# Kernel optimization log

Hardware: AMD Instinct MI355X
Metric: run time of the kernel (lower is better)

The kernel has to match this reference:

```python
import jax, jax.numpy as jnp
import numpy as np

N_HEADS = 16
NEG_INF = -1e30  # stand-in for -inf, safe in fp32/bf16


def setup_inputs() -> dict:
    key = jax.random.key(0)
    k1, k2, k3, k4 = jax.random.split(key, 4)
    B, T, C = 8, 1024, 1024
    x = jax.random.normal(k1, (B, T, C), dtype=jnp.float32)
    # torch nn.Linear weight layout: [out_features, in_features]
    w_attn = jax.random.normal(k2, (3 * C, C), dtype=jnp.float32) * 0.02
    w_proj = jax.random.normal(k3, (C, C), dtype=jnp.float32) * 0.02
    b_proj = jax.random.normal(k4, (C,), dtype=jnp.float32) * 0.02
    return {"x": x, "w_attn": w_attn, "w_proj": w_proj, "b_proj": b_proj}


def reference(x, w_attn, w_proj, b_proj):
    B, T, C = x.shape
    H = N_HEADS
    d = C // H
    # fused QKV projection (bias=False); source splits as keys, queries, values
    qkv = x @ w_attn.T  # [B, T, 3C]
    k, q, v = jnp.split(qkv, 3, axis=-1)
    # [B, T, C] -> [B, H, T, d]
    k = k.reshape(B, T, H, d).transpose(0, 2, 1, 3)
    q = q.reshape(B, T, H, d).transpose(0, 2, 1, 3)
    v = v.reshape(B, T, H, d).transpose(0, 2, 1, 3)
    scale = 1.0 / jnp.sqrt(jnp.asarray(d, dtype=x.dtype))
    att = jnp.einsum('bhqd,bhkd->bhqk', q, k) * scale  # [B, H, T, T]
    causal = jnp.tril(jnp.ones((T, T), dtype=bool))
    att = jnp.where(causal, att, NEG_INF)
    att = jax.nn.softmax(att, axis=-1)
    y = jnp.einsum('bhqk,bhkd->bhqd', att, v)  # [B, H, T, d]
    y = y.transpose(0, 2, 1, 3).reshape(B, T, C)
    return y @ w_proj.T + b_proj
```

## Files before the change

### kernel.cpp

```cpp
#include <hip/hip_runtime.h>
#include <stdint.h>

typedef unsigned short u16;
typedef __attribute__((ext_vector_type(8))) short short8;
typedef __attribute__((ext_vector_type(4))) float f32x4;

__device__ __forceinline__ float bf2f(u16 u) {
    union { unsigned u; float f; } x; x.u = ((unsigned)u) << 16; return x.f;
}
__device__ __forceinline__ float bf_lo(unsigned w) {
    union { unsigned u; float f; } x; x.u = w << 16; return x.f;
}
__device__ __forceinline__ float bf_hi(unsigned w) {
    union { unsigned u; float f; } x; x.u = w & 0xffff0000u; return x.f;
}
__device__ __forceinline__ u16 f2bf(float f) {
    union { float f; unsigned u; } x; x.f = f;
    unsigned r = x.u + 0x7fffu + ((x.u >> 16) & 1u);
    return (u16)(r >> 16);
}
__device__ __forceinline__ uint4 cvt8(const float* p) {
    float4 a = *reinterpret_cast<const float4*>(p);
    float4 b = *reinterpret_cast<const float4*>(p + 4);
    uint4 r;
    r.x = (unsigned)f2bf(a.x) | ((unsigned)f2bf(a.y) << 16);
    r.y = (unsigned)f2bf(a.z) | ((unsigned)f2bf(a.w) << 16);
    r.z = (unsigned)f2bf(b.x) | ((unsigned)f2bf(b.y) << 16);
    r.w = (unsigned)f2bf(b.z) | ((unsigned)f2bf(b.w) << 16);
    return r;
}

__device__ __forceinline__ void gl16(const u16* g, u16* l) {
    __builtin_amdgcn_global_load_lds(
        (const __attribute__((address_space(1))) void*)g,
        (__attribute__((address_space(3))) void*)l, 16, 0, 0);
}

__global__ __launch_bounds__(256) void cvt_kernel(const float* __restrict__ in,
                                                  u16* __restrict__ out, int n8) {
    int i = blockIdx.x * 256 + threadIdx.x;
    if (i < n8) *reinterpret_cast<uint4*>(&out[(size_t)i * 8]) = cvt8(&in[(size_t)i * 8]);
}

#define BM 128
#define BN 128
#define BK 32
#define BKA 64

template<bool CF32>
__global__ __launch_bounds__(256) void gemm_bt_a(const u16* __restrict__ A,
                                                 const u16* __restrict__ W,
                                                 void* __restrict__ Cv,
                                                 const float* __restrict__ bias,
                                                 int M, int N, int K, int lda) {
    __shared__ __align__(16) u16 As[BM * BKA];
    __shared__ __align__(16) u16 Ws[BN * BKA];

    const int tid  = threadIdx.x;
    const int lane = tid & 63;
    const int w    = tid >> 6;
    const int wr   = w >> 1;
    const int wc   = w & 1;
    const int quad = lane >> 4;
    const int l16  = lane & 15;

    const int row0 = blockIdx.y * BM;
    const int col0 = blockIdx.x * BN;

    const int srow = w * 8 + (lane >> 3);
    const int gc   = (lane & 7) ^ (lane >> 3);

    const u16* gA[4]; const u16* gW[4]; u16* lA[4]; u16* lW[4];
#pragma unroll
    for (int p = 0; p < 4; p++) {
        gA[p] = A + (size_t)(row0 + p * 32 + srow) * lda + gc * 8;
        gW[p] = W + (size_t)(col0 + p * 32 + srow) * K  + gc * 8;
        lA[p] = &As[(p * 32 + w * 8) * BKA];
        lW[p] = &Ws[(p * 32 + w * 8) * BKA];
    }

    const int cr0 = ((quad ^ (l16 & 7)) * 8);

    f32x4 acc[4][4] = {};

    for (int k0 = 0; k0 < K; k0 += BKA) {
        __syncthreads();
#pragma unroll
        for (int p = 0; p < 4; p++) {
            gl16(gA[p] + k0, lA[p]);
            gl16(gW[p] + k0, lW[p]);
        }
        __syncthreads();

#pragma unroll
        for (int ks = 0; ks < 2; ks++) {
            const int cc = cr0 ^ (ks * 32);
            short8 af[4], bfr[4];
#pragma unroll
            for (int i = 0; i < 4; i++)
                af[i] = *reinterpret_cast<const short8*>(&As[(wr * 64 + i * 16 + l16) * BKA + cc]);
#pragma unroll
            for (int j = 0; j < 4; j++)
                bfr[j] = *reinterpret_cast<const short8*>(&Ws[(wc * 64 + j * 16 + l16) * BKA + cc]);
#pragma unroll
            for (int i = 0; i < 4; i++)
#pragma unroll
                for (int j = 0; j < 4; j++)
                    acc[i][j] = __builtin_amdgcn_mfma_f32_16x16x32_bf16(af[i], bfr[j], acc[i][j], 0, 0, 0);
        }
    }

#pragma unroll
    for (int j = 0; j < 4; j++) {
        const int col = col0 + wc * 64 + j * 16 + l16;
        const float bval = bias ? bias[col] : 0.0f;
#pragma unroll
        for (int i = 0; i < 4; i++) {
#pragma unroll
            for (int r = 0; r < 4; r++) {
                const int row = row0 + wr * 64 + i * 16 + quad * 4 + r;
                if (CF32) ((float*)Cv)[(size_t)row * N + col] = acc[i][j][r] + bval;
                else      ((u16*)Cv)[(size_t)row * N + col]  = f2bf(acc[i][j][r] + bval);
            }
        }
    }
}

template<bool AF32, bool WF32, bool CF32>
__global__ __launch_bounds__(256) void gemm_bt(const void* __restrict__ Av,
                                               const void* __restrict__ Wv,
                                               void* __restrict__ Cv,
                                               const float* __restrict__ bias,
                                               int M, int N, int K, int lda) {
    __shared__ __align__(16) u16 As[BM * BK];
    __shared__ __align__(16) u16 Ws[BN * BK];

    const int tid  = threadIdx.x;
    const int lane = tid & 63;
    const int wave = tid >> 6;
    const int wr   = wave >> 1;
    const int wc   = wave & 1;
    const int quad = lane >> 4;
    const int l16  = lane & 15;

    const int row0 = blockIdx.y * BM;
    const int col0 = blockIdx.x * BN;

    const int sr = tid >> 2;
    const int sc = (tid & 3) * 8;

    f32x4 acc[4][4] = {};

    for (int k0 = 0; k0 < K; k0 += BK) {
        __syncthreads();
        if (AF32) {
            const float* A = (const float*)Av;
            *reinterpret_cast<uint4*>(&As[(sr)      * BK + sc]) = cvt8(&A[(size_t)(row0 + sr)      * lda + k0 + sc]);
            *reinterpret_cast<uint4*>(&As[(sr + 64) * BK + sc]) = cvt8(&A[(size_t)(row0 + sr + 64) * lda + k0 + sc]);
        } else {
            const u16* A = (const u16*)Av;
            *reinterpret_cast<uint4*>(&As[(sr)      * BK + sc]) =
                *reinterpret_cast<const uint4*>(&A[(size_t)(row0 + sr)      * lda + k0 + sc]);
            *reinterpret_cast<uint4*>(&As[(sr + 64) * BK + sc]) =
                *reinterpret_cast<const uint4*>(&A[(size_t)(row0 + sr + 64) * lda + k0 + sc]);
        }
        if (WF32) {
            const float* W = (const float*)Wv;
            *reinterpret_cast<uint4*>(&Ws[(sr)      * BK + sc]) = cvt8(&W[(size_t)(col0 + sr)      * K + k0 + sc]);
            *reinterpret_cast<uint4*>(&Ws[(sr + 64) * BK + sc]) = cvt8(&W[(size_t)(col0 + sr + 64) * K + k0 + sc]);
        } else {
            const u16* W = (const u16*)Wv;
            *reinterpret_cast<uint4*>(&Ws[(sr)      * BK + sc]) =
                *reinterpret_cast<const uint4*>(&W[(size_t)(col0 + sr)      * K + k0 + sc]);
            *reinterpret_cast<uint4*>(&Ws[(sr + 64) * BK + sc]) =
                *reinterpret_cast<const uint4*>(&W[(size_t)(col0 + sr + 64) * K + k0 + sc]);
        }
        __syncthreads();

        short8 af[4], bfr[4];
#pragma unroll
        for (int i = 0; i < 4; i++)
            af[i] = *reinterpret_cast<const short8*>(&As[(wr * 64 + i * 16 + l16) * BK + quad * 8]);
#pragma unroll
        for (int j = 0; j < 4; j++)
            bfr[j] = *reinterpret_cast<const short8*>(&Ws[(wc * 64 + j * 16 + l16) * BK + quad * 8]);

#pragma unroll
        for (int i = 0; i < 4; i++)
#pragma unroll
            for (int j = 0; j < 4; j++)
                acc[i][j] = __builtin_amdgcn_mfma_f32_16x16x32_bf16(af[i], bfr[j], acc[i][j], 0, 0, 0);
    }

#pragma unroll
    for (int j = 0; j < 4; j++) {
        const int col = col0 + wc * 64 + j * 16 + l16;
        const float bval = bias ? bias[col] : 0.0f;
#pragma unroll
        for (int i = 0; i < 4; i++) {
#pragma unroll
            for (int r = 0; r < 4; r++) {
                const int row = row0 + wr * 64 + i * 16 + quad * 4 + r;
                if (CF32) ((float*)Cv)[(size_t)row * N + col] = acc[i][j][r] + bval;
                else      ((u16*)Cv)[(size_t)row * N + col]  = f2bf(acc[i][j][r] + bval);
            }
        }
    }
}

__global__ __launch_bounds__(256) void vtrans_kernel(const u16* __restrict__ qkv,
                                                     u16* __restrict__ vt) {
    const int bid = blockIdx.x;
    const int tt = bid & 15, h = (bid >> 4) & 15, b = bid >> 8;
    const int t0 = tt * 64;
    __shared__ __align__(16) u16 tile[64 * 72];
    const int tr = threadIdx.x >> 2, tc = (threadIdx.x & 3) * 16;
    const u16* src = qkv + (size_t)(b * 1024 + t0 + tr) * 3072 + 2048 + h * 64 + tc;
    *reinterpret_cast<uint4*>(&tile[tr * 72 + tc])     = *reinterpret_cast<const uint4*>(src);
    *reinterpret_cast<uint4*>(&tile[tr * 72 + tc + 8]) = *reinterpret_cast<const uint4*>(src + 8);
    __syncthreads();
    const int dh = tr, t1 = tc;
    __align__(16) u16 buf[16];
#pragma unroll
    for (int i = 0; i < 16; i++) buf[i] = tile[(t1 + i) * 72 + dh];
    u16* dst = vt + ((size_t)(b * 16 + h) * 64 + dh) * 1024 + t0 + t1;
    *reinterpret_cast<uint4*>(dst)     = *reinterpret_cast<uint4*>(&buf[0]);
    *reinterpret_cast<uint4*>(dst + 8) = *reinterpret_cast<uint4*>(&buf[8]);
}

#define SK 72

__global__ __launch_bounds__(256) void fattn_kernel(u16* __restrict__ qkv,
                                                    const u16* __restrict__ vt) {
    __shared__ __align__(16) u16 Ks[64 * SK];
    __shared__ __align__(16) u16 Vs[64 * SK];
    __shared__ __align__(16) u16 Ps[4][32 * SK];
    __shared__ __align__(16) float aS[4][32];

    const int tid  = threadIdx.x;
    const int lane = tid & 63;
    const int w    = tid >> 6;
    const int quad = lane >> 4;
    const int l16  = lane & 15;

    const int bid = blockIdx.x;
    const int qt  = 7 - (bid >> 7);
    const int bh  = bid & 127;
    const int b   = bh >> 4;
    const int h   = bh & 15;

    u16* qb        = qkv + (size_t)b * 1024 * 3072;
    const u16* vtb = vt + (size_t)bh * 64 * 1024;

    const int qrow0 = qt * 128 + w * 32;

    short8 qf[2][2];
#pragma unroll
    for (int mj = 0; mj < 2; mj++)
#pragma unroll
        for (int ks = 0; ks < 2; ks++) {
            const u16* src = qb + (size_t)(qrow0 + mj * 16 + l16) * 3072 + 1024 + h * 64 + ks * 32 + quad * 8;
            __align__(16) u16 tmp[8];
            *reinterpret_cast<uint4*>(tmp) = *reinterpret_cast<const uint4*>(src);
#pragma unroll
            for (int e = 0; e < 8; e++) tmp[e] = f2bf(bf2f(tmp[e]) * 0.125f);
            qf[mj][ks] = *reinterpret_cast<short8*>(tmp);
        }

    f32x4 oa[2][4] = {};
    float m_run[2] = {-1e30f, -1e30f};
    float l_run[2] = {0.f, 0.f};

    const int jtmax = 2 * qt + 1;
    for (int jt = 0; jt <= jtmax; jt++) {
        const int j0 = jt * 64;
        __syncthreads();
        {
            const int sr = tid >> 2, sc = (tid & 3) * 8;
            const u16* kg = qb + (size_t)(j0 + sr) * 3072 + h * 64;
            *reinterpret_cast<uint4*>(&Ks[sr * SK + sc])      = *reinterpret_cast<const uint4*>(kg + sc);
            *reinterpret_cast<uint4*>(&Ks[sr * SK + sc + 32]) = *reinterpret_cast<const uint4*>(kg + sc + 32);
            const u16* vg = vtb + (size_t)sr * 1024 + j0;
            *reinterpret_cast<uint4*>(&Vs[sr * SK + sc])      = *reinterpret_cast<const uint4*>(vg + sc);
            *reinterpret_cast<uint4*>(&Vs[sr * SK + sc + 32]) = *reinterpret_cast<const uint4*>(vg + sc + 32);
        }
        __syncthreads();

        if (j0 > qrow0 + 31) continue;

        f32x4 s[4][2] = {};
#pragma unroll
        for (int ks = 0; ks < 2; ks++) {
            short8 kf[4];
#pragma unroll
            for (int ti = 0; ti < 4; ti++)
                kf[ti] = *reinterpret_cast<const short8*>(&Ks[(ti * 16 + l16) * SK + ks * 32 + quad * 8]);
#pragma unroll
            for (int ti = 0; ti < 4; ti++)
#pragma unroll
                for (int mj = 0; mj < 2; mj++)
                    s[ti][mj] = __builtin_amdgcn_mfma_f32_16x16x32_bf16(kf[ti], qf[mj][ks], s[ti][mj], 0, 0, 0);
        }

        const bool need_mask = (j0 + 63 > qrow0);
#pragma unroll
        for (int mj = 0; mj < 2; mj++) {
            const int mg = qrow0 + mj * 16 + l16;
            if (need_mask) {
#pragma unroll
                for (int ti = 0; ti < 4; ti++)
#pragma unroll
                    for (int r = 0; r < 4; r++)
                        if (j0 + ti * 16 + quad * 4 + r > mg) s[ti][mj][r] = -1e30f;
            }
            float mt = -1e30f;
#pragma unroll
            for (int ti = 0; ti < 4; ti++)
#pragma unroll
                for (int r = 0; r < 4; r++) mt = fmaxf(mt, s[ti][mj][r]);
            mt = fmaxf(mt, __shfl_xor(mt, 16));
            mt = fmaxf(mt, __shfl_xor(mt, 32));
            const float mn    = fmaxf(m_run[mj], mt);
            const float alpha = __expf(m_run[mj] - mn);
            m_run[mj] = mn;
            float ls = 0.f;
#pragma unroll
            for (int ti = 0; ti < 4; ti++)
#pragma unroll
                for (int r = 0; r < 4; r++) {
                    const float p = __expf(s[ti][mj][r] - mn);
                    s[ti][mj][r] = p;
                    ls += p;
                }
            ls += __shfl_xor(ls, 16);
            ls += __shfl_xor(ls, 32);
            l_run[mj] = l_run[mj] * alpha + ls;
            if (lane < 16) aS[w][mj * 16 + l16] = alpha;
#pragma unroll
            for (int ti = 0; ti < 4; ti++) {
                uint2 pk;
                pk.x = (unsigned)f2bf(s[ti][mj][0]) | ((unsigned)f2bf(s[ti][mj][1]) << 16);
                pk.y = (unsigned)f2bf(s[ti][mj][2]) | ((unsigned)f2bf(s[ti][mj][3]) << 16);
                *reinterpret_cast<uint2*>(&Ps[w][(mj * 16 + l16) * SK + ti * 16 + quad * 4]) = pk;
            }
        }

#pragma unroll
        for (int mi = 0; mi < 2; mi++) {
            const f32x4 av = *reinterpret_cast<const f32x4*>(&aS[w][mi * 16 + quad * 4]);
#pragma unroll
            for (int nd = 0; nd < 4; nd++)
#pragma unroll
                for (int r = 0; r < 4; r++) oa[mi][nd][r] *= av[r];
        }

#pragma unroll
        for (int ks = 0; ks < 2; ks++) {
            short8 pf[2], vf[4];
#pragma unroll
            for (int mi = 0; mi < 2; mi++)
                pf[mi] = *reinterpret_cast<const short8*>(&Ps[w][(mi * 16 + l16) * SK + ks * 32 + quad * 8]);
#pragma unroll
            for (int nd = 0; nd < 4; nd++)
                vf[nd] = *reinterpret_cast<const short8*>(&Vs[(nd * 16 + l16) * SK + ks * 32 + quad * 8]);
#pragma unroll
            for (int mi = 0; mi < 2; mi++)
#pragma unroll
                for (int nd = 0; nd < 4; nd++)
                    oa[mi][nd] = __builtin_amdgcn_mfma_f32_16x16x32_bf16(pf[mi], vf[nd], oa[mi][nd], 0, 0, 0);
        }
    }

    if (lane < 16) { aS[w][l16] = 1.f / l_run[0]; aS[w][16 + l16] = 1.f / l_run[1]; }
#pragma unroll
    for (int mi = 0; mi < 2; mi++) {
        const f32x4 iv = *reinterpret_cast<const f32x4*>(&aS[w][mi * 16 + quad * 4]);
#pragma unroll
        for (int nd = 0; nd < 4; nd++)
#pragma unroll
            for (int r = 0; r < 4; r++) {
                const int row = qrow0 + mi * 16 + quad * 4 + r;
                qb[(size_t)row * 3072 + 1024 + h * 64 + nd * 16 + l16] = f2bf(oa[mi][nd][r] * iv[r]);
            }
    }
}

__global__ __launch_bounds__(256) void attn_kernel(u16* __restrict__ qkv) {
    const int g  = blockIdx.x * 256 + threadIdx.x;
    const int q  = g & 1023;
    const int bh = g >> 10;
    const int b  = bh >> 4;
    const int h  = bh & 15;
    const size_t base = (size_t)b * 1024 * 3072 + (size_t)h * 64;
    float qv[64];
    {
        const uint4* q4 = reinterpret_cast<const uint4*>(qkv + base + (size_t)q * 3072 + 1024);
#pragma unroll
        for (int c = 0; c < 8; c++) {
            uint4 t = q4[c];
            qv[c*8+0]=bf_lo(t.x); qv[c*8+1]=bf_hi(t.x); qv[c*8+2]=bf_lo(t.y); qv[c*8+3]=bf_hi(t.y);
            qv[c*8+4]=bf_lo(t.z); qv[c*8+5]=bf_hi(t.z); qv[c*8+6]=bf_lo(t.w); qv[c*8+7]=bf_hi(t.w);
        }
    }
    float o[64];
#pragma unroll
    for (int i = 0; i < 64; i++) o[i] = 0.0f;
    float m = -1e30f, l = 0.0f;
    const int jmax = q | 63;
    for (int j = 0; j <= jmax; j++) {
        const uint4* k4 = reinterpret_cast<const uint4*>(qkv + base + (size_t)j * 3072);
        float s = 0.0f;
#pragma unroll
        for (int c = 0; c < 8; c++) {
            uint4 t = k4[c];
            s += qv[c*8+0]*bf_lo(t.x)+qv[c*8+1]*bf_hi(t.x)+qv[c*8+2]*bf_lo(t.y)+qv[c*8+3]*bf_hi(t.y)
               + qv[c*8+4]*bf_lo(t.z)+qv[c*8+5]*bf_hi(t.z)+qv[c*8+6]*bf_lo(t.w)+qv[c*8+7]*bf_hi(t.w);
        }
        s *= 0.125f;
        const bool act = (j <= q);
        if (!act) s = -1e30f;
        const float mn = fmaxf(m, s);
        const float alpha = __expf(m - mn);
        float p = __expf(s - mn);
        if (!act) p = 0.0f;
        l = l * alpha + p;
        const uint4* v4 = reinterpret_cast<const uint4*>(qkv + base + (size_t)j * 3072 + 2048);
#pragma unroll
        for (int c = 0; c < 8; c++) {
            uint4 t = v4[c];
            o[c*8+0]=o[c*8+0]*alpha+p*bf_lo(t.x); o[c*8+1]=o[c*8+1]*alpha+p*bf_hi(t.x);
            o[c*8+2]=o[c*8+2]*alpha+p*bf_lo(t.y); o[c*8+3]=o[c*8+3]*alpha+p*bf_hi(t.y);
            o[c*8+4]=o[c*8+4]*alpha+p*bf_lo(t.z); o[c*8+5]=o[c*8+5]*alpha+p*bf_hi(t.z);
            o[c*8+6]=o[c*8+6]*alpha+p*bf_lo(t.w); o[c*8+7]=o[c*8+7]*alpha+p*bf_hi(t.w);
        }
        m = mn;
    }
    const float inv = 1.0f / l;
    u16* yrow = qkv + base + (size_t)q * 3072 + 1024;
#pragma unroll
    for (int i = 0; i < 64; i++) yrow[i] = f2bf(o[i] * inv);
}

extern "C" void kernel_launch(void* const* d_in, const int* in_sizes, int n_in,
                              void* d_out, int out_size, void* d_ws, size_t ws_size,
                              hipStream_t stream) {
    const float* x      = (const float*)d_in[0];
    const float* w_attn = (const float*)d_in[1];
    const float* w_proj = (const float*)d_in[2];
    const float* b_proj = (const float*)d_in[3];
    float* out = (float*)d_out;

    const int M = 8192, K = 1024;
    const size_t QKV = (size_t)8192 * 3072;
    const size_t VT  = (size_t)8 * 16 * 64 * 1024;

    u16* qkv = (u16*)d_ws;
    u16* vtb = qkv + QKV;
    u16* xb  = vtb + VT;
    u16* wab = xb + (size_t)8192 * 1024;
    u16* wpb = wab + (size_t)3072 * 1024;

    const size_t need_full = (QKV + VT + (size_t)8192*1024 + (size_t)3072*1024 + (size_t)1024*1024) * 2;
    const size_t need_mid  = (QKV + VT) * 2;

    if (ws_size >= need_full) {
        cvt_kernel<<<4096, 256, 0, stream>>>(x, xb, 8192 * 1024 / 8);
        cvt_kernel<<<1536, 256, 0, stream>>>(w_attn, wab, 3072 * 1024 / 8);
        cvt_kernel<<<512,  256, 0, stream>>>(w_proj, wpb, 1024 * 1024 / 8);
        gemm_bt_a<false><<<dim3(24, 64), 256, 0, stream>>>(xb, wab, qkv, nullptr, M, 3072, K, K);
        vtrans_kernel<<<2048, 256, 0, stream>>>(qkv, vtb);
        fattn_kernel<<<1024, 256, 0, stream>>>(qkv, vtb);
        gemm_bt_a<true><<<dim3(8, 64), 256, 0, stream>>>(qkv + 1024, wpb, out, b_proj, M, 1024, K, 3072);
    } else if (ws_size >= need_mid) {
        gemm_bt<true, true, false><<<dim3(24, 64), 256, 0, stream>>>(x, w_attn, qkv, nullptr, M, 3072, K, K);
        vtrans_kernel<<<2048, 256, 0, stream>>>(qkv, vtb);
        fattn_kernel<<<1024, 256, 0, stream>>>(qkv, vtb);
        gemm_bt<false, true, true><<<dim3(8, 64), 256, 0, stream>>>(qkv + 1024, w_proj, out, b_proj, M, 1024, K, 3072);
    } else {
        gemm_bt<true, true, false><<<dim3(24, 64), 256, 0, stream>>>(x, w_attn, qkv, nullptr, M, 3072, K, K);
        attn_kernel<<<512, 256, 0, stream>>>(qkv);
        gemm_bt<false, true, true><<<dim3(8, 64), 256, 0, stream>>>(qkv + 1024, w_proj, out, b_proj, M, 1024, K, 3072);
    }
}
```

Measured before the change: 247.5 us.

## Fuse V transpose into QKV GEMM, double-buffer LDS, merge conversion kernels

```diff
diff --git a/kernel.cpp b/kernel.cpp
--- a/kernel.cpp
+++ b/kernel.cpp
@@ -42,6 +42,19 @@
     if (i < n8) *reinterpret_cast<uint4*>(&out[(size_t)i * 8]) = cvt8(&in[(size_t)i * 8]);
 }
 
+__global__ __launch_bounds__(256) void cvt3_kernel(const float* __restrict__ a, int na8,
+                                                   const float* __restrict__ b, int nb8,
+                                                   const float* __restrict__ c, int nc8,
+                                                   u16* __restrict__ dst) {
+    int i = blockIdx.x * 256 + threadIdx.x;
+    const float* src; int off;
+    if (i < na8)            { src = a; off = i; }
+    else if (i < na8 + nb8) { src = b; off = i - na8; }
+    else if (i < na8 + nb8 + nc8) { src = c; off = i - na8 - nb8; }
+    else return;
+    *reinterpret_cast<uint4*>(&dst[(size_t)i * 8]) = cvt8(&src[(size_t)off * 8]);
+}
+
 #define BM 128
 #define BN 128
 #define BK 32
@@ -52,9 +65,10 @@
                                                  const u16* __restrict__ W,
                                                  void* __restrict__ Cv,
                                                  const float* __restrict__ bias,
-                                                 int M, int N, int K, int lda) {
-    __shared__ __align__(16) u16 As[BM * BKA];
-    __shared__ __align__(16) u16 Ws[BN * BKA];
+                                                 int M, int N, int K, int lda,
+                                                 u16* __restrict__ vt) {
+    __shared__ __align__(16) u16 As[2][BM * BKA];
+    __shared__ __align__(16) u16 Ws[2][BN * BKA];
 
     const int tid  = threadIdx.x;
     const int lane = tid & 63;
@@ -70,27 +84,35 @@
     const int srow = w * 8 + (lane >> 3);
     const int gc   = (lane & 7) ^ (lane >> 3);
 
-    const u16* gA[4]; const u16* gW[4]; u16* lA[4]; u16* lW[4];
+    const u16* gA[4]; const u16* gW[4];
 #pragma unroll
     for (int p = 0; p < 4; p++) {
         gA[p] = A + (size_t)(row0 + p * 32 + srow) * lda + gc * 8;
         gW[p] = W + (size_t)(col0 + p * 32 + srow) * K  + gc * 8;
-        lA[p] = &As[(p * 32 + w * 8) * BKA];
-        lW[p] = &Ws[(p * 32 + w * 8) * BKA];
-    }
-
-    const int cr0 = ((quad ^ (l16 & 7)) * 8);
+    }
+    const int lofs = (w * 8) * BKA;
+
+    const int cr0 = (quad ^ (l16 & 7)) * 8;
 
     f32x4 acc[4][4] = {};
 
+#pragma unroll
+    for (int p = 0; p < 4; p++) {
+        gl16(gA[p], &As[0][p * 32 * BKA + lofs]);
+        gl16(gW[p], &Ws[0][p * 32 * BKA + lofs]);
+    }
+
+    int cur = 0;
     for (int k0 = 0; k0 < K; k0 += BKA) {
         __syncthreads();
-#pragma unroll
-        for (int p = 0; p < 4; p++) {
-            gl16(gA[p] + k0, lA[p]);
-            gl16(gW[p] + k0, lW[p]);
-        }
-        __syncthreads();
+        if (k0 + BKA < K) {
+            const int nxt = cur ^ 1;
+#pragma unroll
+            for (int p = 0; p < 4; p++) {
+                gl16(gA[p] + k0 + BKA, &As[nxt][p * 32 * BKA + lofs]);
+                gl16(gW[p] + k0 + BKA, &Ws[nxt][p * 32 * BKA + lofs]);
+            }
+        }
 
 #pragma unroll
         for (int ks = 0; ks < 2; ks++) {
@@ -98,29 +120,47 @@
             short8 af[4], bfr[4];
 #pragma unroll
             for (int i = 0; i < 4; i++)
-                af[i] = *reinterpret_cast<const short8*>(&As[(wr * 64 + i * 16 + l16) * BKA + cc]);
+                af[i] = *reinterpret_cast<const short8*>(&As[cur][(wr * 64 + i * 16 + l16) * BKA + cc]);
 #pragma unroll
             for (int j = 0; j < 4; j++)
-                bfr[j] = *reinterpret_cast<const short8*>(&Ws[(wc * 64 + j * 16 + l16) * BKA + cc]);
+                bfr[j] = *reinterpret_cast<const short8*>(&Ws[cur][(wc * 64 + j * 16 + l16) * BKA + cc]);
 #pragma unroll
             for (int i = 0; i < 4; i++)
 #pragma unroll
                 for (int j = 0; j < 4; j++)
                     acc[i][j] = __builtin_amdgcn_mfma_f32_16x16x32_bf16(af[i], bfr[j], acc[i][j], 0, 0, 0);
         }
-    }
-
-#pragma unroll
-    for (int j = 0; j < 4; j++) {
-        const int col = col0 + wc * 64 + j * 16 + l16;
-        const float bval = bias ? bias[col] : 0.0f;
-#pragma unroll
-        for (int i = 0; i < 4; i++) {
-#pragma unroll
-            for (int r = 0; r < 4; r++) {
-                const int row = row0 + wr * 64 + i * 16 + quad * 4 + r;
-                if (CF32) ((float*)Cv)[(size_t)row * N + col] = acc[i][j][r] + bval;
-                else      ((u16*)Cv)[(size_t)row * N + col]  = f2bf(acc[i][j][r] + bval);
+        cur ^= 1;
+    }
+
+    if (vt != nullptr && col0 >= 2048) {
+        const int b = row0 >> 10;
+#pragma unroll
+        for (int j = 0; j < 4; j++) {
+            const int hd = col0 - 2048 + wc * 64 + j * 16 + l16;
+            u16* dstc = vt + (size_t)(b * 1024 + hd) * 1024 + (row0 & 1023) + wr * 64;
+#pragma unroll
+            for (int i = 0; i < 4; i++) {
+                const int t0 = i * 16 + quad * 4;
+                u16 pk[4];
+#pragma unroll
+                for (int r = 0; r < 4; r++) pk[r] = f2bf(acc[i][j][r]);
+                *reinterpret_cast<uint2*>(dstc + t0) = *reinterpret_cast<uint2*>(pk);
+            }
+        }
+    } else {
+#pragma unroll
+        for (int j = 0; j < 4; j++) {
+            const int col = col0 + wc * 64 + j * 16 + l16;
+            const float bval = bias ? bias[col] : 0.0f;
+#pragma unroll
+            for (int i = 0; i < 4; i++) {
+#pragma unroll
+                for (int r = 0; r < 4; r++) {
+                    const int row = row0 + wr * 64 + i * 16 + quad * 4 + r;
+                    if (CF32) ((float*)Cv)[(size_t)row * N + col] = acc[i][j][r] + bval;
+                    else      ((u16*)Cv)[(size_t)row * N + col]  = f2bf(acc[i][j][r] + bval);
+                }
             }
         }
     }
@@ -464,13 +504,12 @@
     const size_t need_mid  = (QKV + VT) * 2;
 
     if (ws_size >= need_full) {
-        cvt_kernel<<<4096, 256, 0, stream>>>(x, xb, 8192 * 1024 / 8);
-        cvt_kernel<<<1536, 256, 0, stream>>>(w_attn, wab, 3072 * 1024 / 8);
-        cvt_kernel<<<512,  256, 0, stream>>>(w_proj, wpb, 1024 * 1024 / 8);
-        gemm_bt_a<false><<<dim3(24, 64), 256, 0, stream>>>(xb, wab, qkv, nullptr, M, 3072, K, K);
-        vtrans_kernel<<<2048, 256, 0, stream>>>(qkv, vtb);
+        cvt3_kernel<<<6144, 256, 0, stream>>>(x, 8192 * 1024 / 8,
+                                              w_attn, 3072 * 1024 / 8,
+                                              w_proj, 1024 * 1024 / 8, xb);
+        gemm_bt_a<false><<<dim3(24, 64), 256, 0, stream>>>(xb, wab, qkv, nullptr, M, 3072, K, K, vtb);
         fattn_kernel<<<1024, 256, 0, stream>>>(qkv, vtb);
-        gemm_bt_a<true><<<dim3(8, 64), 256, 0, stream>>>(qkv + 1024, wpb, out, b_proj, M, 1024, K, 3072);
+        gemm_bt_a<true><<<dim3(8, 64), 256, 0, stream>>>(qkv + 1024, wpb, out, b_proj, M, 1024, K, 3072, nullptr);
     } else if (ws_size >= need_mid) {
         gemm_bt<true, true, false><<<dim3(24, 64), 256, 0, stream>>>(x, w_attn, qkv, nullptr, M, 3072, K, K);
         vtrans_kernel<<<2048, 256, 0, stream>>>(qkv, vtb);
```

After: 234.7 us. 1.05x faster.
